# Performance work log

Measured on AMD Instinct MI355X. Metric: run time of the kernel, lower is better.

Reference implementation:

```python
import jax, jax.numpy as jnp
import numpy as np

B, LQ, LK = 8, 2048, 2048
D_IN, D_KQ, D_OUT = 512, 512, 512


def setup_inputs() -> dict:
    key = jax.random.key(0)
    ks = jax.random.split(key, 8)
    s = 0.02
    return {
        "x_1": jax.random.normal(ks[0], (B, LQ, D_IN), jnp.float32),
        "x_2": jax.random.normal(ks[1], (B, LK, D_IN), jnp.float32),
        "Wq": jax.random.normal(ks[2], (D_IN, D_KQ), jnp.float32) * s,
        "bq": jax.random.normal(ks[3], (D_KQ,), jnp.float32) * s,
        "Wk": jax.random.normal(ks[4], (D_IN, D_KQ), jnp.float32) * s,
        "bk": jax.random.normal(ks[5], (D_KQ,), jnp.float32) * s,
        "Wv": jax.random.normal(ks[6], (D_IN, D_OUT), jnp.float32) * s,
        "bv": jax.random.normal(ks[7], (D_OUT,), jnp.float32) * s,
    }


def reference(x_1, x_2, Wq, bq, Wk, bk, Wv, bv):
    q = x_1 @ Wq + bq                      # [B, LQ, D_KQ]
    k = x_2 @ Wk + bk                      # [B, LK, D_KQ]
    v = x_2 @ Wv + bv                      # [B, LK, D_OUT]
    scores = jnp.einsum('bqd,bkd->bqk', q, k) / jnp.sqrt(jnp.float32(D_KQ))
    attn = jax.nn.softmax(scores, axis=-1)  # [B, LQ, LK]
    return jnp.einsum('bqk,bkd->bqd', attn, v)
```

## Files before the change

### kernel.cpp

```cpp
#include <hip/hip_runtime.h>
#include <hip/hip_bf16.h>
#include <stdint.h>

typedef __attribute__((ext_vector_type(8))) short bf16x8;
typedef __attribute__((ext_vector_type(4))) float f32x4;

#define MFMA16(a, b, c) __builtin_amdgcn_mfma_f32_16x16x32_bf16((a), (b), (c), 0, 0, 0)

__device__ __forceinline__ unsigned short f2bf(float f) {
    union { float f; uint32_t u; } c; c.f = f;
    uint32_t u = c.u + 0x7fffu + ((c.u >> 16) & 1u);
    return (unsigned short)(u >> 16);
}

__device__ __forceinline__ void gll16(const void* g, void* l) {
    __builtin_amdgcn_global_load_lds((const __attribute__((address_space(1))) void*)g,
                                     (__attribute__((address_space(3))) void*)l, 16, 0, 0);
}

__global__ void wtrans_kernel(const float* __restrict__ Wq, const float* __restrict__ Wk,
                              const float* __restrict__ Wv,
                              unsigned short* __restrict__ WqT, unsigned short* __restrict__ WkT,
                              unsigned short* __restrict__ WvT) {
    __shared__ float tile[32][33];
    const int z = blockIdx.z;
    const float* W = (z == 0) ? Wq : ((z == 1) ? Wk : Wv);
    unsigned short* WT = (z == 0) ? WqT : ((z == 1) ? WkT : WvT);
    const int k0 = blockIdx.x * 32, n0 = blockIdx.y * 32;
    const int tx = threadIdx.x, ty = threadIdx.y;
#pragma unroll
    for (int i = ty; i < 32; i += 8)
        tile[i][tx] = W[(size_t)(k0 + i) * 512 + n0 + tx];
    __syncthreads();
#pragma unroll
    for (int i = ty; i < 32; i += 8)
        WT[(size_t)(n0 + i) * 512 + k0 + tx] = f2bf(tile[tx][i]);
}

__global__ __launch_bounds__(512) void proj_kernel(
        const float* __restrict__ x1, const float* __restrict__ x2,
        const unsigned short* __restrict__ WqT, const unsigned short* __restrict__ WkT,
        const unsigned short* __restrict__ WvT,
        const float* __restrict__ bq, const float* __restrict__ bk, const float* __restrict__ bv,
        unsigned short* __restrict__ Qb, unsigned short* __restrict__ Kb,
        unsigned short* __restrict__ Vtb) {
    __shared__ __align__(16) char psm[36864];
    char* As = psm;
    char* Bs = psm + 4096;

    const int z = blockIdx.y;
    const float* X = (z == 0) ? x1 : x2;
    const unsigned short* WT = (z == 0) ? WqT : ((z == 1) ? WkT : WvT);
    const float* bias = (z == 0) ? bq : ((z == 1) ? bk : bv);

    const int tid = threadIdx.x, w = tid >> 6, lane = tid & 63;
    const int l15 = lane & 15, g = lane >> 4;
    const int mb = blockIdx.x * 64;

    const int swA = ((l15 >> 1) & 3) << 4;
    const int bsrc_col = ((lane & 3) * 16) ^ (((lane >> 3) & 3) << 4);

    f32x4 acc[4][4] = {};

    for (int kt = 0; kt < 16; ++kt) {
        const int k0 = kt * 32;
        {
            const int m = tid >> 3, fc = (tid & 7) * 4;
            const float4 v = *(const float4*)(X + (size_t)(mb + m) * 512 + k0 + fc);
            ushort4 b4;
            b4.x = f2bf(v.x); b4.y = f2bf(v.y); b4.z = f2bf(v.z); b4.w = f2bf(v.w);
            *(ushort4*)(As + m * 64 + (((tid & 7) * 8) ^ (((m >> 1) & 3) << 4))) = b4;
        }
#pragma unroll
        for (int c = 0; c < 4; ++c) {
            const int n = w * 64 + c * 16 + (lane >> 2);
            gll16((const char*)WT + (size_t)n * 1024 + k0 * 2 + bsrc_col,
                  Bs + w * 4096 + c * 1024);
        }
        asm volatile("s_waitcnt vmcnt(0)" ::: "memory");
        __syncthreads();

        bf16x8 af[4], bfr[4];
#pragma unroll
        for (int r2 = 0; r2 < 4; ++r2)
            af[r2] = *(const bf16x8*)(As + (r2 * 16 + l15) * 64 + ((g * 16) ^ swA));
#pragma unroll
        for (int cb = 0; cb < 4; ++cb)
            bfr[cb] = *(const bf16x8*)(Bs + (w * 64 + cb * 16 + l15) * 64 + ((g * 16) ^ swA));
#pragma unroll
        for (int r2 = 0; r2 < 4; ++r2)
#pragma unroll
            for (int cb = 0; cb < 4; ++cb)
                acc[r2][cb] = MFMA16(af[r2], bfr[cb], acc[r2][cb]);
        __syncthreads();
    }

#pragma unroll
    for (int cb = 0; cb < 4; ++cb) {
        const int n = w * 64 + cb * 16 + l15;
        const float bn = bias[n];
#pragma unroll
        for (int r2 = 0; r2 < 4; ++r2) {
#pragma unroll
            for (int r = 0; r < 4; ++r) {
                const int row = r2 * 16 + g * 4 + r;
                const float val = acc[r2][cb][r] + bn;
                const unsigned short o = f2bf(val);
                if (z == 0) {
                    Qb[(size_t)(mb + row) * 512 + n] = o;
                } else if (z == 1) {
                    Kb[(size_t)(mb + row) * 512 + n] = o;
                } else {
                    const int gm = mb + row;
                    Vtb[((size_t)(gm >> 11) * 512 + n) * 2048 + (gm & 2047)] = o;
                }
            }
        }
    }
}

#define ATTN_SCALE 0.04419417382415922f
#define ATTN_LDS_BYTES 139776

__global__ __attribute__((amdgpu_waves_per_eu(2, 2))) __launch_bounds__(512)
void attn_kernel(const unsigned short* __restrict__ Q,
                 const unsigned short* __restrict__ K,
                 const unsigned short* __restrict__ Vt,
                 float* __restrict__ out) {
    extern __shared__ __align__(16) char smem[];
    char* Ps = smem + 131072;
    float* lred = (float*)(smem + 139264);

    const int tid = threadIdx.x, w = tid >> 6, lane = tid & 63;
    const int l15 = lane & 15, g = lane >> 4;
    const int b = blockIdx.x, q0 = blockIdx.y * 64;
    const int rb = w >> 1, cbq = w & 1;
    const int qb4 = rb * 16 + g * 4;

    const char* Kg = (const char*)K + (size_t)b * 2048 * 1024;
    const char* Vg = (const char*)Vt + (size_t)b * 512 * 4096;

    const int vsrc_col = ((lane & 3) * 16) ^ (((lane >> 3) & 3) << 4);
    const int krow = cbq * 16 + l15;
    const int ksw = (krow & 7) << 4;
    const int psw = (l15 & 7) << 4;
    const int vsw = ((l15 >> 1) & 3) << 4;

    auto stage = [&](int kt, int cur) {
        char* kb = smem + (cur << 15);
        char* vb = smem + 65536 + (cur << 15);
        const char* kg = Kg + (size_t)kt * 32768;
        const char* vg = Vg + (size_t)kt * 64;
#pragma unroll
        for (int c = 0; c < 4; ++c) {
            const int r = w * 4 + c;
            gll16(kg + (size_t)r * 1024 + ((lane * 16) ^ ((r & 7) << 4)), kb + r * 1024);
            const int dv = w * 64 + c * 16 + (lane >> 2);
            gll16(vg + (size_t)dv * 4096 + vsrc_col, vb + w * 4096 + c * 1024);
        }
    };

    stage(0, 0);

    bf16x8 qreg[16];
    {
        const char* qrow = (const char*)Q + ((size_t)b * 2048 + q0 + rb * 16 + l15) * 1024;
#pragma unroll
        for (int dk = 0; dk < 16; ++dk)
            qreg[dk] = *(const bf16x8*)(qrow + dk * 64 + g * 16);
    }

    f32x4 acc[4][4] = {};
    float lsum[4] = {0.f, 0.f, 0.f, 0.f};

    for (int kt = 0; kt < 64; ++kt) {
        const int cur = kt & 1;
        asm volatile("s_waitcnt vmcnt(0)" ::: "memory");
        __syncthreads();
        if (kt < 63) stage(kt + 1, cur ^ 1);

        const char* kb = smem + (cur << 15) + krow * 1024;
        f32x4 sA = {}, sB = {};
#pragma unroll
        for (int dk = 0; dk < 8; ++dk) {
            bf16x8 kf = *(const bf16x8*)(kb + ((dk * 64 + g * 16) ^ ksw));
            sA = MFMA16(qreg[dk], kf, sA);
        }
#pragma unroll
        for (int dk = 8; dk < 16; ++dk) {
            bf16x8 kf = *(const bf16x8*)(kb + ((dk * 64 + g * 16) ^ ksw));
            sB = MFMA16(qreg[dk], kf, sB);
        }
#pragma unroll
        for (int r = 0; r < 4; ++r) {
            const float p = __expf((sA[r] + sB[r]) * ATTN_SCALE);
            lsum[r] += p;
            const int q = qb4 + r;
            *(unsigned short*)(Ps + q * 128 + (((cbq * 16 + l15) * 2) ^ ((q & 7) << 4))) = f2bf(p);
        }

        asm volatile("s_waitcnt lgkmcnt(0)" ::: "memory");
        __builtin_amdgcn_s_barrier();
        __builtin_amdgcn_sched_barrier(0);
        asm volatile("" ::: "memory");

        const char* vbb = smem + 65536 + (cur << 15);
        bf16x8 pa[4];
#pragma unroll
        for (int r2 = 0; r2 < 4; ++r2)
            pa[r2] = *(const bf16x8*)(Ps + (r2 * 16 + l15) * 128 + ((g * 16) ^ psw));
#pragma unroll
        for (int cb = 0; cb < 4; ++cb) {
            const int dv = w * 64 + cb * 16 + l15;
            bf16x8 vf = *(const bf16x8*)(vbb + dv * 64 + ((g * 16) ^ vsw));
#pragma unroll
            for (int r2 = 0; r2 < 4; ++r2)
                acc[r2][cb] = MFMA16(pa[r2], vf, acc[r2][cb]);
        }
    }

#pragma unroll
    for (int r = 0; r < 4; ++r) {
        float v = lsum[r];
        v += __shfl_xor(v, 1); v += __shfl_xor(v, 2);
        v += __shfl_xor(v, 4); v += __shfl_xor(v, 8);
        lsum[r] = v;
    }
    if (l15 == 0) {
#pragma unroll
        for (int r = 0; r < 4; ++r) lred[cbq * 64 + qb4 + r] = lsum[r];
    }
    __syncthreads();

    float* outb = out + ((size_t)b * 2048 + q0) * 512 + w * 64;
#pragma unroll
    for (int r2 = 0; r2 < 4; ++r2) {
#pragma unroll
        for (int r = 0; r < 4; ++r) {
            const int q = r2 * 16 + g * 4 + r;
            const float linv = 1.0f / (lred[q] + lred[64 + q]);
#pragma unroll
            for (int cb = 0; cb < 4; ++cb)
                outb[(size_t)q * 512 + cb * 16 + l15] = acc[r2][cb][r] * linv;
        }
    }
}

extern "C" void kernel_launch(void* const* d_in, const int* in_sizes, int n_in,
                              void* d_out, int out_size, void* d_ws, size_t ws_size,
                              hipStream_t stream) {
    const float* x1 = (const float*)d_in[0];
    const float* x2 = (const float*)d_in[1];
    const float* Wq = (const float*)d_in[2];
    const float* bq = (const float*)d_in[3];
    const float* Wk = (const float*)d_in[4];
    const float* bk = (const float*)d_in[5];
    const float* Wv = (const float*)d_in[6];
    const float* bv = (const float*)d_in[7];
    float* out = (float*)d_out;

    char* ws = (char*)d_ws;
    unsigned short* Qb  = (unsigned short*)(ws);
    unsigned short* Kb  = (unsigned short*)(ws + 16777216);
    unsigned short* Vtb = (unsigned short*)(ws + 33554432);
    unsigned short* WqT = (unsigned short*)(ws + 50331648);
    unsigned short* WkT = (unsigned short*)(ws + 50331648 + 524288);
    unsigned short* WvT = (unsigned short*)(ws + 50331648 + 1048576);

    wtrans_kernel<<<dim3(16, 16, 3), dim3(32, 8), 0, stream>>>(Wq, Wk, Wv, WqT, WkT, WvT);

    proj_kernel<<<dim3(256, 3), 512, 0, stream>>>(x1, x2, WqT, WkT, WvT,
                                                  bq, bk, bv, Qb, Kb, Vtb);

    hipFuncSetAttribute((const void*)attn_kernel,
                        hipFuncAttributeMaxDynamicSharedMemorySize, ATTN_LDS_BYTES);
    attn_kernel<<<dim3(8, 32), 512, ATTN_LDS_BYTES, stream>>>(Qb, Kb, Vtb, out);
}
```

Before: 291.2 us.

## Restructure projection and attention kernels with larger tiles and pipelined loads

The projection kernel now uses a 64x256 tile over a 2D N split, with K steps of 64 and a software pipeline. X values are prefetched into registers and W is double-buffered through direct global-to-LDS loads. The V transpose is staged through LDS so stores are coalesced 16-byte writes. The attention kernel moves to 64-key tiles: each wave holds Q fragments for two 16-row blocks, K and V loads are interleaved with the QK and PV phases under split barriers, and row sums are reduced across four column groups. This aims to cut barrier count, improve global-store coalescing and raise MFMA density, at the cost of more registers and LDS and more complex waitcnt ordering.

```diff
diff --git a/kernel.cpp b/kernel.cpp
--- a/kernel.cpp
+++ b/kernel.cpp
@@ -44,83 +44,138 @@
         const float* __restrict__ bq, const float* __restrict__ bk, const float* __restrict__ bv,
         unsigned short* __restrict__ Qb, unsigned short* __restrict__ Kb,
         unsigned short* __restrict__ Vtb) {
-    __shared__ __align__(16) char psm[36864];
-    char* As = psm;
-    char* Bs = psm + 4096;
-
-    const int z = blockIdx.y;
+    extern __shared__ __align__(16) char psm[];
+    const int z = blockIdx.z;
     const float* X = (z == 0) ? x1 : x2;
     const unsigned short* WT = (z == 0) ? WqT : ((z == 1) ? WkT : WvT);
     const float* bias = (z == 0) ? bq : ((z == 1) ? bk : bv);
 
     const int tid = threadIdx.x, w = tid >> 6, lane = tid & 63;
     const int l15 = lane & 15, g = lane >> 4;
-    const int mb = blockIdx.x * 64;
-
-    const int swA = ((l15 >> 1) & 3) << 4;
-    const int bsrc_col = ((lane & 3) * 16) ^ (((lane >> 3) & 3) << 4);
-
-    f32x4 acc[4][4] = {};
-
-    for (int kt = 0; kt < 16; ++kt) {
-        const int k0 = kt * 32;
-        {
-            const int m = tid >> 3, fc = (tid & 7) * 4;
-            const float4 v = *(const float4*)(X + (size_t)(mb + m) * 512 + k0 + fc);
-            ushort4 b4;
-            b4.x = f2bf(v.x); b4.y = f2bf(v.y); b4.z = f2bf(v.z); b4.w = f2bf(v.w);
-            *(ushort4*)(As + m * 64 + (((tid & 7) * 8) ^ (((m >> 1) & 3) << 4))) = b4;
-        }
-#pragma unroll
-        for (int c = 0; c < 4; ++c) {
-            const int n = w * 64 + c * 16 + (lane >> 2);
-            gll16((const char*)WT + (size_t)n * 1024 + k0 * 2 + bsrc_col,
-                  Bs + w * 4096 + c * 1024);
-        }
-        asm volatile("s_waitcnt vmcnt(0)" ::: "memory");
-        __syncthreads();
-
-        bf16x8 af[4], bfr[4];
-#pragma unroll
-        for (int r2 = 0; r2 < 4; ++r2)
-            af[r2] = *(const bf16x8*)(As + (r2 * 16 + l15) * 64 + ((g * 16) ^ swA));
-#pragma unroll
-        for (int cb = 0; cb < 4; ++cb)
-            bfr[cb] = *(const bf16x8*)(Bs + (w * 64 + cb * 16 + l15) * 64 + ((g * 16) ^ swA));
-#pragma unroll
-        for (int r2 = 0; r2 < 4; ++r2)
-#pragma unroll
-            for (int cb = 0; cb < 4; ++cb)
-                acc[r2][cb] = MFMA16(af[r2], bfr[cb], acc[r2][cb]);
-        __syncthreads();
-    }
-
-#pragma unroll
-    for (int cb = 0; cb < 4; ++cb) {
-        const int n = w * 64 + cb * 16 + l15;
-        const float bn = bias[n];
-#pragma unroll
-        for (int r2 = 0; r2 < 4; ++r2) {
-#pragma unroll
-            for (int r = 0; r < 4; ++r) {
-                const int row = r2 * 16 + g * 4 + r;
-                const float val = acc[r2][cb][r] + bn;
-                const unsigned short o = f2bf(val);
-                if (z == 0) {
-                    Qb[(size_t)(mb + row) * 512 + n] = o;
-                } else if (z == 1) {
-                    Kb[(size_t)(mb + row) * 512 + n] = o;
-                } else {
-                    const int gm = mb + row;
-                    Vtb[((size_t)(gm >> 11) * 512 + n) * 2048 + (gm & 2047)] = o;
+    const int mb = blockIdx.x * 64, nb = blockIdx.y * 256;
+
+    const int xm = tid >> 3, xk8 = (tid & 7) * 8;
+    const int awcol = ((tid & 7) * 16) ^ (((tid >> 3) & 7) << 4);
+    const int wcol = ((lane & 7) * 16) ^ (((lane >> 3) & 7) << 4);
+    const int l7x16 = (l15 & 7) << 4;
+
+    const float* Xrow = X + (size_t)(mb + xm) * 512 + xk8;
+    const char* Wbase = (const char*)WT + (size_t)(nb + (lane >> 3)) * 1024 + wcol;
+
+    f32x4 acc[4][2] = {};
+    float4 xr0[2], xr1[2];
+
+    xr0[0] = *(const float4*)(Xrow);
+    xr0[1] = *(const float4*)(Xrow + 4);
+#pragma unroll
+    for (int c = 0; c < 4; ++c)
+        gll16(Wbase + (size_t)(w * 32 + c * 8) * 1024,
+              psm + 16384 + (w * 32 + c * 8) * 128);
+
+#define PROJ_STEP(KT, XC, XN, AOFF, BOFF, BNOFF)                               \
+    {                                                                          \
+        if ((KT) < 7) {                                                        \
+            const float* xs = Xrow + ((KT) + 1) * 64;                          \
+            XN[0] = *(const float4*)xs;                                        \
+            XN[1] = *(const float4*)(xs + 4);                                  \
+            _Pragma("unroll")                                                  \
+            for (int c = 0; c < 4; ++c)                                        \
+                gll16(Wbase + ((KT) + 1) * 128 + (size_t)(w * 32 + c * 8) * 1024, \
+                      psm + (BNOFF) + (w * 32 + c * 8) * 128);                 \
+            asm volatile("s_waitcnt vmcnt(6)" ::: "memory");                   \
+        } else {                                                               \
+            asm volatile("s_waitcnt vmcnt(0)" ::: "memory");                   \
+        }                                                                      \
+        {                                                                      \
+            uint32_t p0 = f2bf(XC[0].x) | ((uint32_t)f2bf(XC[0].y) << 16);     \
+            uint32_t p1 = f2bf(XC[0].z) | ((uint32_t)f2bf(XC[0].w) << 16);     \
+            uint32_t p2 = f2bf(XC[1].x) | ((uint32_t)f2bf(XC[1].y) << 16);     \
+            uint32_t p3 = f2bf(XC[1].z) | ((uint32_t)f2bf(XC[1].w) << 16);     \
+            int4 av; av.x = p0; av.y = p1; av.z = p2; av.w = p3;               \
+            *(int4*)(psm + (AOFF) + xm * 128 + awcol) = av;                    \
+        }                                                                      \
+        asm volatile("s_waitcnt lgkmcnt(0)" ::: "memory");                     \
+        __builtin_amdgcn_sched_barrier(0);                                     \
+        __builtin_amdgcn_s_barrier();                                          \
+        __builtin_amdgcn_sched_barrier(0);                                     \
+        _Pragma("unroll")                                                      \
+        for (int ks = 0; ks < 2; ++ks) {                                       \
+            bf16x8 af[4], bfr[2];                                              \
+            _Pragma("unroll")                                                  \
+            for (int rb = 0; rb < 4; ++rb)                                     \
+                af[rb] = *(const bf16x8*)(psm + (AOFF) + (rb * 16 + l15) * 128 \
+                                          + ((ks * 64 + g * 16) ^ l7x16));     \
+            _Pragma("unroll")                                                  \
+            for (int cb = 0; cb < 2; ++cb)                                     \
+                bfr[cb] = *(const bf16x8*)(psm + (BOFF)                        \
+                           + (w * 32 + cb * 16 + l15) * 128                    \
+                           + ((ks * 64 + g * 16) ^ l7x16));                    \
+            _Pragma("unroll")                                                  \
+            for (int rb = 0; rb < 4; ++rb)                                     \
+                _Pragma("unroll")                                              \
+                for (int cb = 0; cb < 2; ++cb)                                 \
+                    acc[rb][cb] = MFMA16(af[rb], bfr[cb], acc[rb][cb]);        \
+        }                                                                      \
+        __builtin_amdgcn_sched_barrier(0);                                     \
+        __builtin_amdgcn_s_barrier();                                          \
+        __builtin_amdgcn_sched_barrier(0);                                     \
+    }
+
+    PROJ_STEP(0, xr0, xr1, 0,    16384, 49152)
+    PROJ_STEP(1, xr1, xr0, 8192, 49152, 16384)
+    PROJ_STEP(2, xr0, xr1, 0,    16384, 49152)
+    PROJ_STEP(3, xr1, xr0, 8192, 49152, 16384)
+    PROJ_STEP(4, xr0, xr1, 0,    16384, 49152)
+    PROJ_STEP(5, xr1, xr0, 8192, 49152, 16384)
+    PROJ_STEP(6, xr0, xr1, 0,    16384, 49152)
+    PROJ_STEP(7, xr1, xr0, 8192, 49152, 16384)
+#undef PROJ_STEP
+
+    if (z < 2) {
+        unsigned short* O = (z == 0) ? Qb : Kb;
+#pragma unroll
+        for (int cb = 0; cb < 2; ++cb) {
+            const int n = nb + w * 32 + cb * 16 + l15;
+            const float bn = bias[n];
+#pragma unroll
+            for (int rb = 0; rb < 4; ++rb)
+#pragma unroll
+                for (int r = 0; r < 4; ++r)
+                    O[(size_t)(mb + rb * 16 + g * 4 + r) * 512 + n] =
+                        f2bf(acc[rb][cb][r] + bn);
+        }
+    } else {
+        char* Tr = psm;
+#pragma unroll
+        for (int cb = 0; cb < 2; ++cb) {
+            const int nl = w * 32 + cb * 16 + l15;
+            const float bn = bias[nb + nl];
+#pragma unroll
+            for (int rb = 0; rb < 4; ++rb)
+#pragma unroll
+                for (int r = 0; r < 4; ++r) {
+                    const int m2 = (rb * 16 + g * 4 + r) * 2;
+                    *(unsigned short*)(Tr + nl * 128 + (m2 ^ l7x16)) =
+                        f2bf(acc[rb][cb][r] + bn);
                 }
-            }
+        }
+        asm volatile("s_waitcnt lgkmcnt(0)" ::: "memory");
+        __builtin_amdgcn_sched_barrier(0);
+        __builtin_amdgcn_s_barrier();
+        __builtin_amdgcn_sched_barrier(0);
+        const int bidx = mb >> 11, kv0 = mb & 2047;
+#pragma unroll
+        for (int it = 0; it < 4; ++it) {
+            const int idx = it * 512 + tid;
+            const int n2 = idx >> 3, t8 = idx & 7;
+            int4 v = *(const int4*)(Tr + n2 * 128 + ((t8 * 16) ^ ((n2 & 7) << 4)));
+            *(int4*)(Vtb + ((size_t)bidx * 512 + nb + n2) * 2048 + kv0 + t8 * 8) = v;
         }
     }
 }
 
 #define ATTN_SCALE 0.04419417382415922f
-#define ATTN_LDS_BYTES 139776
+#define ATTN_LDS_BYTES 140288
 
 __global__ __attribute__((amdgpu_waves_per_eu(2, 2))) __launch_bounds__(512)
 void attn_kernel(const unsigned short* __restrict__ Q,
@@ -128,122 +183,150 @@
                  const unsigned short* __restrict__ Vt,
                  float* __restrict__ out) {
     extern __shared__ __align__(16) char smem[];
+    char* Kb = smem;
+    char* Vb = smem + 65536;
     char* Ps = smem + 131072;
     float* lred = (float*)(smem + 139264);
 
     const int tid = threadIdx.x, w = tid >> 6, lane = tid & 63;
     const int l15 = lane & 15, g = lane >> 4;
-    const int b = blockIdx.x, q0 = blockIdx.y * 64;
-    const int rb = w >> 1, cbq = w & 1;
-    const int qb4 = rb * 16 + g * 4;
+    const int b = blockIdx.x, qb0 = blockIdx.y * 64;
+    const int rb2 = w >> 2, cb4 = w & 3;
+    const int l7x16 = (l15 & 7) << 4;
 
     const char* Kg = (const char*)K + (size_t)b * 2048 * 1024;
     const char* Vg = (const char*)Vt + (size_t)b * 512 * 4096;
-
-    const int vsrc_col = ((lane & 3) * 16) ^ (((lane >> 3) & 3) << 4);
-    const int krow = cbq * 16 + l15;
-    const int ksw = (krow & 7) << 4;
-    const int psw = (l15 & 7) << 4;
-    const int vsw = ((l15 >> 1) & 3) << 4;
-
-    auto stage = [&](int kt, int cur) {
-        char* kb = smem + (cur << 15);
-        char* vb = smem + 65536 + (cur << 15);
-        const char* kg = Kg + (size_t)kt * 32768;
-        const char* vg = Vg + (size_t)kt * 64;
-#pragma unroll
-        for (int c = 0; c < 4; ++c) {
-            const int r = w * 4 + c;
-            gll16(kg + (size_t)r * 1024 + ((lane * 16) ^ ((r & 7) << 4)), kb + r * 1024);
-            const int dv = w * 64 + c * 16 + (lane >> 2);
-            gll16(vg + (size_t)dv * 4096 + vsrc_col, vb + w * 4096 + c * 1024);
-        }
-    };
-
-    stage(0, 0);
-
-    bf16x8 qreg[16];
+    const int vcol = ((lane & 7) * 16) ^ (((lane >> 3) & 7) << 4);
+    const int vrow = lane >> 3;
+
     {
-        const char* qrow = (const char*)Q + ((size_t)b * 2048 + q0 + rb * 16 + l15) * 1024;
-#pragma unroll
-        for (int dk = 0; dk < 16; ++dk)
-            qreg[dk] = *(const bf16x8*)(qrow + dk * 64 + g * 16);
+        const char* kg = Kg;
+#pragma unroll
+        for (int c = 0; c < 8; ++c) {
+            const int r = w * 8 + c;
+            gll16(kg + (size_t)r * 1024 + ((lane * 16) ^ (c << 4)), Kb + r * 1024);
+        }
+    }
+    bf16x8 qreg[2][16];
+    {
+        const char* qbase = (const char*)Q +
+            ((size_t)b * 2048 + qb0 + rb2 * 32 + l15) * 1024 + g * 16;
+#pragma unroll
+        for (int qb = 0; qb < 2; ++qb)
+#pragma unroll
+            for (int ks = 0; ks < 16; ++ks)
+                qreg[qb][ks] = *(const bf16x8*)(qbase + qb * 16384 + ks * 64);
     }
 
     f32x4 acc[4][4] = {};
-    float lsum[4] = {0.f, 0.f, 0.f, 0.f};
-
-    for (int kt = 0; kt < 64; ++kt) {
-        const int cur = kt & 1;
+    float lsum[2][4] = {};
+
+    for (int kt = 0; kt < 32; ++kt) {
         asm volatile("s_waitcnt vmcnt(0)" ::: "memory");
-        __syncthreads();
-        if (kt < 63) stage(kt + 1, cur ^ 1);
-
-        const char* kb = smem + (cur << 15) + krow * 1024;
-        f32x4 sA = {}, sB = {};
-#pragma unroll
-        for (int dk = 0; dk < 8; ++dk) {
-            bf16x8 kf = *(const bf16x8*)(kb + ((dk * 64 + g * 16) ^ ksw));
-            sA = MFMA16(qreg[dk], kf, sA);
-        }
-#pragma unroll
-        for (int dk = 8; dk < 16; ++dk) {
-            bf16x8 kf = *(const bf16x8*)(kb + ((dk * 64 + g * 16) ^ ksw));
-            sB = MFMA16(qreg[dk], kf, sB);
-        }
+        __builtin_amdgcn_sched_barrier(0);
+        __builtin_amdgcn_s_barrier();
+        __builtin_amdgcn_sched_barrier(0);
+
+        {
+            const char* vg = Vg + (size_t)kt * 128;
+#pragma unroll
+            for (int c = 0; c < 8; ++c) {
+                const int r0 = w * 64 + c * 8;
+                gll16(vg + (size_t)(r0 + vrow) * 4096 + vcol, Vb + r0 * 128);
+            }
+        }
+
+        const char* kbr = Kb + (cb4 * 16 + l15) * 1024;
+        f32x4 s0 = {}, s1 = {};
+#pragma unroll
+        for (int ks = 0; ks < 16; ++ks) {
+            bf16x8 kf = *(const bf16x8*)(kbr + ((ks * 64 + g * 16) ^ l7x16));
+            s0 = MFMA16(qreg[0][ks], kf, s0);
+            s1 = MFMA16(qreg[1][ks], kf, s1);
+        }
+
+        __builtin_amdgcn_sched_barrier(0);
+        __builtin_amdgcn_s_barrier();
+        __builtin_amdgcn_sched_barrier(0);
+
+        {
+            const char* kg = Kg + (size_t)((kt + 1) & 31) * 65536;
+#pragma unroll
+            for (int c = 0; c < 8; ++c) {
+                const int r = w * 8 + c;
+                gll16(kg + (size_t)r * 1024 + ((lane * 16) ^ (c << 4)), Kb + r * 1024);
+            }
+        }
+
 #pragma unroll
         for (int r = 0; r < 4; ++r) {
-            const float p = __expf((sA[r] + sB[r]) * ATTN_SCALE);
-            lsum[r] += p;
-            const int q = qb4 + r;
-            *(unsigned short*)(Ps + q * 128 + (((cbq * 16 + l15) * 2) ^ ((q & 7) << 4))) = f2bf(p);
-        }
-
+            const float p0 = __expf(s0[r] * ATTN_SCALE);
+            const float p1 = __expf(s1[r] * ATTN_SCALE);
+            lsum[0][r] += p0;
+            lsum[1][r] += p1;
+            const int q0r = rb2 * 32 + g * 4 + r;
+            const int xk = ((q0r & 7) << 4);
+            const int cc = (cb4 * 16 + l15) * 2;
+            *(unsigned short*)(Ps + q0r * 128 + (cc ^ xk)) = f2bf(p0);
+            *(unsigned short*)(Ps + (q0r + 16) * 128 + (cc ^ xk)) = f2bf(p1);
+        }
+
+        asm volatile("s_waitcnt vmcnt(8)" ::: "memory");
         asm volatile("s_waitcnt lgkmcnt(0)" ::: "memory");
+        __builtin_amdgcn_sched_barrier(0);
         __builtin_amdgcn_s_barrier();
         __builtin_amdgcn_sched_barrier(0);
-        asm volatile("" ::: "memory");
-
-        const char* vbb = smem + 65536 + (cur << 15);
-        bf16x8 pa[4];
-#pragma unroll
-        for (int r2 = 0; r2 < 4; ++r2)
-            pa[r2] = *(const bf16x8*)(Ps + (r2 * 16 + l15) * 128 + ((g * 16) ^ psw));
-#pragma unroll
-        for (int cb = 0; cb < 4; ++cb) {
-            const int dv = w * 64 + cb * 16 + l15;
-            bf16x8 vf = *(const bf16x8*)(vbb + dv * 64 + ((g * 16) ^ vsw));
-#pragma unroll
-            for (int r2 = 0; r2 < 4; ++r2)
-                acc[r2][cb] = MFMA16(pa[r2], vf, acc[r2][cb]);
-        }
-    }
-
-#pragma unroll
-    for (int r = 0; r < 4; ++r) {
-        float v = lsum[r];
-        v += __shfl_xor(v, 1); v += __shfl_xor(v, 2);
-        v += __shfl_xor(v, 4); v += __shfl_xor(v, 8);
-        lsum[r] = v;
-    }
+
+#pragma unroll
+        for (int ks2 = 0; ks2 < 2; ++ks2) {
+            bf16x8 pa[4];
+#pragma unroll
+            for (int qb = 0; qb < 4; ++qb)
+                pa[qb] = *(const bf16x8*)(Ps + (qb * 16 + l15) * 128 +
+                                          ((ks2 * 64 + g * 16) ^ l7x16));
+#pragma unroll
+            for (int dvb = 0; dvb < 4; ++dvb) {
+                bf16x8 vf = *(const bf16x8*)(Vb + (w * 64 + dvb * 16 + l15) * 128 +
+                                             ((ks2 * 64 + g * 16) ^ l7x16));
+#pragma unroll
+                for (int qb = 0; qb < 4; ++qb)
+                    acc[qb][dvb] = MFMA16(pa[qb], vf, acc[qb][dvb]);
+            }
+        }
+    }
+
+    asm volatile("s_waitcnt vmcnt(0)" ::: "memory");
+
+#pragma unroll
+    for (int qb = 0; qb < 2; ++qb)
+#pragma unroll
+        for (int r = 0; r < 4; ++r) {
+            float v = lsum[qb][r];
+            v += __shfl_xor(v, 1); v += __shfl_xor(v, 2);
+            v += __shfl_xor(v, 4); v += __shfl_xor(v, 8);
+            lsum[qb][r] = v;
+        }
     if (l15 == 0) {
 #pragma unroll
-        for (int r = 0; r < 4; ++r) lred[cbq * 64 + qb4 + r] = lsum[r];
+        for (int qb = 0; qb < 2; ++qb)
+#pragma unroll
+            for (int r = 0; r < 4; ++r)
+                lred[cb4 * 64 + rb2 * 32 + qb * 16 + g * 4 + r] = lsum[qb][r];
     }
     __syncthreads();
 
-    float* outb = out + ((size_t)b * 2048 + q0) * 512 + w * 64;
-#pragma unroll
-    for (int r2 = 0; r2 < 4; ++r2) {
+    float* outb = out + ((size_t)b * 2048 + qb0) * 512 + w * 64;
+#pragma unroll
+    for (int qb = 0; qb < 4; ++qb)
 #pragma unroll
         for (int r = 0; r < 4; ++r) {
-            const int q = r2 * 16 + g * 4 + r;
-            const float linv = 1.0f / (lred[q] + lred[64 + q]);
-#pragma unroll
-            for (int cb = 0; cb < 4; ++cb)
-                outb[(size_t)q * 512 + cb * 16 + l15] = acc[r2][cb][r] * linv;
-        }
-    }
+            const int q = qb * 16 + g * 4 + r;
+            const float linv =
+                1.0f / (lred[q] + lred[64 + q] + lred[128 + q] + lred[192 + q]);
+#pragma unroll
+            for (int dvb = 0; dvb < 4; ++dvb)
+                outb[(size_t)q * 512 + dvb * 16 + l15] = acc[qb][dvb][r] * linv;
+        }
 }
 
 extern "C" void kernel_launch(void* const* d_in, const int* in_sizes, int n_in,
@@ -269,8 +352,10 @@
 
     wtrans_kernel<<<dim3(16, 16, 3), dim3(32, 8), 0, stream>>>(Wq, Wk, Wv, WqT, WkT, WvT);
 
-    proj_kernel<<<dim3(256, 3), 512, 0, stream>>>(x1, x2, WqT, WkT, WvT,
-                                                  bq, bk, bv, Qb, Kb, Vtb);
+    hipFuncSetAttribute((const void*)proj_kernel,
+                        hipFuncAttributeMaxDynamicSharedMemorySize, 81920);
+    proj_kernel<<<dim3(256, 2, 3), 512, 81920, stream>>>(x1, x2, WqT, WkT, WvT,
+                                                         bq, bk, bv, Qb, Kb, Vtb);
 
     hipFuncSetAttribute((const void*)attn_kernel,
                         hipFuncAttributeMaxDynamicSharedMemorySize, ATTN_LDS_BYTES);
```

After: 474.5 us. 1.63x slower.
